# Performance work log

Hardware: AMD Instinct MI355X
Metric: run time of the kernel (lower is better)

Reference implementation:

```python
import jax, jax.numpy as jnp
import numpy as np

MODEL_DIM = 128
N_FRAMES = 128
N_SAMPLES = 32768
N_TABLES = 8
TABLE_SIZE = 512
BATCH = 8
N_FREQS = 16


def _mlp(x, w1, b1, w2, b2, w3, b3):
    # LinearOutputStack(channels, 3, ...): Linear -> lrelu -> Linear -> lrelu -> Linear
    h = jax.nn.leaky_relu(x @ w1 + b1, 0.2)
    h = jax.nn.leaky_relu(h @ w2 + b2, 0.2)
    return h @ w3 + b3


def _pos_encoded(t, n_freqs=N_FREQS):
    # (t, 1 + 2*n_freqs) = (t, 33): raw position plus sin/cos at geometric freqs
    pos = jnp.linspace(-1.0, 1.0, t, dtype=jnp.float32)
    scales = (2.0 ** jnp.arange(n_freqs, dtype=jnp.float32)) * jnp.pi
    ang = pos[:, None] * scales[None, :]
    return jnp.concatenate([pos[:, None], jnp.sin(ang), jnp.cos(ang)], axis=-1)


def _interp_linear(env, out_size):
    # torch F.interpolate(mode='linear', align_corners=False) from (B, F) to (B, out_size)
    f = env.shape[-1]
    coord = (jnp.arange(out_size, dtype=jnp.float32) + 0.5) * (f / out_size) - 0.5
    i0 = jnp.floor(coord)
    frac = (coord - i0).astype(env.dtype)
    i0c = jnp.clip(i0, 0, f - 1).astype(jnp.int32)
    i1c = jnp.clip(i0 + 1, 0, f - 1).astype(jnp.int32)
    return env[:, i0c] * (1.0 - frac) + env[:, i1c] * frac


def setup_inputs() -> dict:
    key = jax.random.key(0)
    ks = jax.random.split(key, 16)
    wi = 0.02  # weight_init from Experiment
    d = MODEL_DIM

    def lin(k, i, o):
        return jax.random.normal(k, (i, o), jnp.float32) * wi

    inp = {
        "x": jax.random.normal(ks[0], (BATCH, d), jnp.float32),
        "wavetables": jax.random.uniform(ks[1], (N_TABLES, TABLE_SIZE), jnp.float32, -1.0, 1.0),
    }
    specs = {"tc": (d, N_TABLES), "env": (d, N_FRAMES), "pos": (33, d), "sk": (d, TABLE_SIZE)}
    i = 2
    for name, (cin, cout) in specs.items():
        k1, k2, k3 = jax.random.split(ks[i], 3)
        inp[f"{name}_w1"] = lin(k1, cin, d)
        inp[f"{name}_b1"] = jnp.zeros((d,), jnp.float32)
        inp[f"{name}_w2"] = lin(k2, d, d)
        inp[f"{name}_b2"] = jnp.zeros((d,), jnp.float32)
        inp[f"{name}_w3"] = lin(k3, d, cout)
        inp[f"{name}_b3"] = jnp.zeros((cout,), jnp.float32)
        i += 1
    return inp


def reference(x, wavetables,
              tc_w1, tc_b1, tc_w2, tc_b2, tc_w3, tc_b3,
              env_w1, env_b1, env_w2, env_b2, env_w3, env_b3,
              pos_w1, pos_b1, pos_w2, pos_b2, pos_w3, pos_b3,
              sk_w1, sk_b1, sk_w2, sk_b2, sk_w3, sk_b3):
    # table choice: softmax then hard max (straight value * gathered table)
    c = jax.nn.softmax(_mlp(x, tc_w1, tc_b1, tc_w2, tc_b2, tc_w3, tc_b3), axis=-1)
    values = jnp.max(c, axis=-1)          # (B,)
    indices = jnp.argmax(c, axis=-1)      # (B,)

    mx = jnp.max(wavetables, axis=-1, keepdims=True)
    wt = wavetables / (mx + 1e-8)
    sel = wt[indices]                     # (B, TABLE_SIZE)

    env = jnp.abs(_mlp(x, env_w1, env_b1, env_w2, env_b2, env_w3, env_b3))  # (B, N_FRAMES)
    env = _interp_linear(env, N_SAMPLES)  # (B, N_SAMPLES)

    # pos encoding is identical across batch; embed once then broadcast (same math)
    pe = _pos_encoded(N_SAMPLES)          # (T, 33)
    pos = _mlp(pe, pos_w1, pos_b1, pos_w2, pos_b2, pos_w3, pos_b3)  # (T, D)
    pos = pos[None, :, :] + x[:, None, :]  # (B, T, D)

    sk = jax.nn.softmax(_mlp(pos, sk_w1, sk_b1, sk_w2, sk_b2, sk_w3, sk_b3), axis=-1)  # (B, T, K)

    # selected_tables (B,1,K) @ kernel^T (B,K,T) -> (B,1,T)
    sampled = jnp.einsum('bk,btk->bt', sel, sk)
    sampled = sampled * env * values[:, None]
    return sampled[:, None, :]
```

## Files before the change

### kernel.cpp

```cpp
#include <hip/hip_runtime.h>
#include <math.h>

#define D 128
#define B 8
#define T_SAMP 32768
#define K 512
#define NT 8
#define NFRM 128

#define WS_C1   0
#define WS_ENV8 1024
#define WS_SEL  2048
#define WS_VAL  6144
#define WS_B3P  6160
#define WSBF_BYTE 32768
#define FP1 0
#define FP2 8192
#define FP3 24576
#define FS1 40960
#define FS2 57344
#define FS3 73728
#define WTOT 139264
#define WS_NEED (WSBF_BYTE + WTOT*2)

typedef __attribute__((ext_vector_type(8))) short short8;
typedef __attribute__((ext_vector_type(4))) float f32x4;

#define LOG2E 1.4426950408889634f

__device__ __forceinline__ float lrelu(float v){ return fmaxf(v, 0.2f*v); }

__device__ __forceinline__ unsigned cvtpk(float lo, float hi){
    unsigned r;
    asm("v_cvt_pk_bf16_f32 %0, %1, %2" : "=v"(r) : "v"(lo), "v"(hi));
    return r;
}
__device__ __forceinline__ unsigned short bfr(float f){
    unsigned u = __builtin_bit_cast(unsigned, f); u += 0x7fffu + ((u>>16)&1u);
    return (unsigned short)(u>>16);
}
__device__ __forceinline__ float bf2f(short s){
    unsigned u = ((unsigned)(unsigned short)s) << 16;
    return __builtin_bit_cast(float, u);
}
__device__ __forceinline__ float exp2fast(float x){
#if __has_builtin(__builtin_amdgcn_exp2f)
    return __builtin_amdgcn_exp2f(x);
#else
    return __expf(x*0.6931471805599453f);
#endif
}
__device__ __forceinline__ float sin_rev(float fr){
#if __has_builtin(__builtin_amdgcn_sinf)
    return __builtin_amdgcn_sinf(fr);
#else
    return __sinf(fr*6.283185307179586f);
#endif
}
__device__ __forceinline__ float cos_rev(float fr){
#if __has_builtin(__builtin_amdgcn_cosf)
    return __builtin_amdgcn_cosf(fr);
#else
    return __cosf(fr*6.283185307179586f);
#endif
}
__device__ __forceinline__ float pe_val(float pf, int j){
    if (j == 0) return pf;
    if (j > 32) return 0.f;
    const bool is_sin = (j <= 16);
    int e = is_sin ? (j + 125) : (j + 109);
    float sc = __builtin_bit_cast(float, ((unsigned)e) << 23);
    float u = pf * sc;
    float fr = u - floorf(u);
    return is_sin ? sin_rev(fr) : cos_rev(fr);
}

#define VMCNT0 asm volatile("s_waitcnt vmcnt(0)" ::: "memory")

__device__ void layer128(const float* __restrict__ in, const float* __restrict__ w,
                         const float* __restrict__ bias, float* __restrict__ outp,
                         int tid, int mode)
{
    int n = tid & 127, bg = tid >> 7;
    const float* i0 = in + (bg*4+0)*D;
    const float* i1 = in + (bg*4+1)*D;
    const float* i2 = in + (bg*4+2)*D;
    const float* i3 = in + (bg*4+3)*D;
    float bb = bias[n];
    float a0=bb,a1=bb,a2=bb,a3=bb;
    #pragma unroll 4
    for (int j=0;j<D;j++){
        float wv = w[j*D+n];
        a0 = fmaf(i0[j], wv, a0);
        a1 = fmaf(i1[j], wv, a1);
        a2 = fmaf(i2[j], wv, a2);
        a3 = fmaf(i3[j], wv, a3);
    }
    if (mode==0){ a0=lrelu(a0);a1=lrelu(a1);a2=lrelu(a2);a3=lrelu(a3); }
    else if (mode==1){ a0=fabsf(a0);a1=fabsf(a1);a2=fabsf(a2);a3=fabsf(a3); }
    outp[(bg*4+0)*D+n]=a0;
    outp[(bg*4+1)*D+n]=a1;
    outp[(bg*4+2)*D+n]=a2;
    outp[(bg*4+3)*D+n]=a3;
}

__global__ __launch_bounds__(256) void setup_kernel(
    const float* __restrict__ x, const float* __restrict__ wt,
    const float* __restrict__ tc_w1, const float* __restrict__ tc_b1,
    const float* __restrict__ tc_w2, const float* __restrict__ tc_b2,
    const float* __restrict__ tc_w3, const float* __restrict__ tc_b3,
    const float* __restrict__ env_w1, const float* __restrict__ env_b1,
    const float* __restrict__ env_w2, const float* __restrict__ env_b2,
    const float* __restrict__ env_w3, const float* __restrict__ env_b3,
    const float* __restrict__ sk_w1, const float* __restrict__ sk_b1,
    const float* __restrict__ pos_w1, const float* __restrict__ pos_w2,
    const float* __restrict__ pos_w3, const float* __restrict__ sk_w2,
    const float* __restrict__ sk_w3, const float* __restrict__ sk_b3,
    float* __restrict__ ws)
{
    __shared__ float xl[B*D], buf1[B*D], buf2[B*D];
    __shared__ float lgts[B*NT], pmax[NT*8], mxr[NT];
    __shared__ int idxl[B];
    int tid = threadIdx.x;

    if (blockIdx.x >= 2){
        int idx = (blockIdx.x - 2)*256 + tid;
        if (idx >= WTOT) return;
        unsigned short* wb = (unsigned short*)((char*)ws + WSBF_BYTE);
        int r; const float* Wp; int ncols = D; int nkt = 4; bool p1 = false;
        if (idx < FP2){ r = idx - FP1; Wp = pos_w1; nkt = 2; p1 = true; }
        else if (idx < FP3){ r = idx - FP2; Wp = pos_w2; }
        else if (idx < FS1){ r = idx - FP3; Wp = pos_w3; }
        else if (idx < FS2){ r = idx - FS1; Wp = sk_w1; }
        else if (idx < FS3){ r = idx - FS2; Wp = sk_w2; }
        else { r = idx - FS3; Wp = sk_w3; ncols = K; }
        int frag = r >> 9, lane = (r >> 3) & 63, e = r & 7;
        int nt2 = frag / nkt, kt = frag - nt2*nkt;
        int k = 32*kt + 8*(lane>>4) + e;
        int n = 16*nt2 + (lane&15);
        float v = (p1 && k >= 33) ? 0.f : Wp[k*ncols + n];
        wb[idx] = bfr(v);
        return;
    }

    for (int i=tid;i<B*D;i+=256) xl[i]=x[i];
    __syncthreads();

    if (blockIdx.x == 1){
        for (int i=tid;i<K;i+=256) ws[WS_B3P+i] = sk_b3[i]*LOG2E;
        layer128(xl, env_w1, env_b1, buf1, tid, 0);
        __syncthreads();
        layer128(buf1, env_w2, env_b2, buf2, tid, 0);
        __syncthreads();
        layer128(buf2, env_w3, env_b3, ws+WS_ENV8, tid, 1);
        layer128(xl, sk_w1, sk_b1, ws+WS_C1, tid, 2);
        return;
    }

    layer128(xl, tc_w1, tc_b1, buf1, tid, 0);
    __syncthreads();
    layer128(buf1, tc_w2, tc_b2, buf2, tid, 0);
    __syncthreads();
    if (tid < 64){
        int b = tid>>3, n = tid&7;
        float a = tc_b3[n];
        #pragma unroll 4
        for (int j=0;j<D;j++) a = fmaf(buf2[b*D+j], tc_w3[j*NT+n], a);
        lgts[b*NT+n] = a;
    } else if (tid < 128){
        int r = (tid-64)>>3, p = tid&7;
        float m = -1e30f;
        for (int k=p*64;k<p*64+64;k++) m = fmaxf(m, wt[r*K+k]);
        pmax[r*8+p] = m;
    }
    __syncthreads();
    if (tid < 8){
        int b = tid; float m = -1e30f; int idx = 0;
        for (int n=0;n<NT;n++){ float v = lgts[b*NT+n]; if (v > m){ m=v; idx=n; } }
        float S = 0.f;
        for (int n=0;n<NT;n++) S += expf(lgts[b*NT+n]-m);
        ws[WS_VAL+b] = 1.0f/S;
        idxl[b] = idx;
    } else if (tid < 16){
        int r = tid-8; float m = -1e30f;
        for (int p=0;p<8;p++) m = fmaxf(m, pmax[r*8+p]);
        mxr[r] = m;
    }
    __syncthreads();
    for (int o=tid;o<B*K;o+=256){
        int b = o>>9, k = o&(K-1);
        int id = idxl[b];
        ws[WS_SEL+o] = wt[id*K+k] / (mxr[id] + 1e-8f);
    }
}

template<int NKT_IN, bool ACT>
__device__ __forceinline__ void layerF(const short8* aw,
                                       const unsigned char* inb, unsigned char* outb,
                                       const float* biasp, int wv, int lg, int lc)
{
    const f32x4 z = {0.f,0.f,0.f,0.f};
    const int lane16 = (lg*16 + lc)*16;
    const int obase = ((wv>>1)<<10) + (((2*(wv&1) + (lg>>1))*16 + lc)<<4) + ((lg&1)<<3);
    f32x4 bb = z;
    if (biasp) bb = *(const f32x4*)(biasp + 16*wv + 4*lg);
    #pragma unroll
    for (int rt=0;rt<2;rt++){
        f32x4 d = z;
        #pragma unroll
        for (int kt=0;kt<NKT_IN;kt++){
            short8 bf = *(const short8*)(inb + ((rt*NKT_IN+kt)<<10) + lane16);
            d = __builtin_amdgcn_mfma_f32_16x16x32_bf16(aw[kt], bf, d, 0,0,0);
        }
        float o0 = d[0]+bb[0], o1 = d[1]+bb[1], o2 = d[2]+bb[2], o3 = d[3]+bb[3];
        if (ACT){ o0=lrelu(o0); o1=lrelu(o1); o2=lrelu(o2); o3=lrelu(o3); }
        uint2 u; u.x = cvtpk(o0,o1); u.y = cvtpk(o2,o3);
        *(uint2*)(outb + (rt<<12) + obase) = u;
    }
}

__global__ __launch_bounds__(512, 4) void synth7(
    const float* __restrict__ pos_b1, const float* __restrict__ pos_b2,
    const float* __restrict__ pos_b3, const float* __restrict__ sk_b2,
    const float* __restrict__ ws, float* __restrict__ out)
{
    __shared__ __align__(16) unsigned char lds[32768];
    unsigned char* abA = lds;
    unsigned char* abB = lds + 8192;
    unsigned char* PEb = abB;

    const int tid = threadIdx.x;
    const int wv = tid >> 6, lane = tid & 63, lg = lane >> 4, lc = lane & 15;
    const int lane16 = lane*16;
    const int t0 = blockIdx.x * 32;
    const unsigned short* wg16 = (const unsigned short*)((const char*)ws + WSBF_BYTE);
    const f32x4 z = {0.f,0.f,0.f,0.f};

    auto stage = [&](int elemoff, unsigned char* dst, int nchunks){
        const unsigned char* src = (const unsigned char*)(wg16 + elemoff);
        for (int c = wv; c < nchunks; c += 8)
            __builtin_amdgcn_global_load_lds(
                (const __attribute__((address_space(1))) unsigned int*)(src + (c<<10) + lane16),
                (__attribute__((address_space(3))) unsigned int*)(dst + (c<<10)), 16, 0, 0);
    };

    short8 aw1[2];
    #pragma unroll
    for (int kt=0;kt<2;kt++)
        aw1[kt] = *(const short8*)(wg16 + FP1 + ((wv*2+kt)<<9) + lane*8);
    for (int i = tid; i < 1024; i += 512){
        int r = i >> 5, p = i & 31;
        int j0 = 2*p;
        float pf = (float)(-1.0 + 2.0*(double)(t0+r)/32767.0);
        float v0 = pe_val(pf, j0);
        float v1 = pe_val(pf, j0+1);
        int kt = j0 >> 5, rem = j0 & 31;
        int by = (((r>>4)*2 + kt)<<10) + (((rem>>3)*16 + (r&15))<<4) + (rem&7)*2;
        *(unsigned*)(PEb + by) = cvtpk(v0, v1);
    }
    __syncthreads();

    short8 awn[4];
    #pragma unroll
    for (int kt=0;kt<4;kt++)
        awn[kt] = *(const short8*)(wg16 + FP2 + ((wv*4+kt)<<9) + lane*8);
    layerF<2,true>(aw1, PEb, abA, pos_b1, wv, lg, lc);
    __syncthreads();
    {
        short8 awp[4];
        #pragma unroll
        for (int kt=0;kt<4;kt++)
            awp[kt] = *(const short8*)(wg16 + FP3 + ((wv*4+kt)<<9) + lane*8);
        layerF<4,true>(awn, abA, abB, pos_b2, wv, lg, lc);
        #pragma unroll
        for (int kt=0;kt<4;kt++) awn[kt] = awp[kt];
    }
    __syncthreads();
    {
        short8 awp[4];
        #pragma unroll
        for (int kt=0;kt<4;kt++)
            awp[kt] = *(const short8*)(wg16 + FS1 + ((wv*4+kt)<<9) + lane*8);
        layerF<4,false>(awn, abB, abA, pos_b3, wv, lg, lc);
        #pragma unroll
        for (int kt=0;kt<4;kt++) awn[kt] = awp[kt];
    }
    __syncthreads();
    layerF<4,false>(awn, abA, abB, nullptr, wv, lg, lc);
    __syncthreads();

    stage(FS2, lds, 8);
    short8 hf[2][4];
    {
        const int b = lc & 7;
        const float* c1g = ws + WS_C1 + b*128;
        #pragma unroll
        for (int rtl=0;rtl<2;rtl++){
            int tl = 4*wv + 2*rtl + (lc>>3);
            int fr = tl >> 4, lrow = tl & 15;
            #pragma unroll
            for (int kt=0;kt<4;kt++){
                short8 a1v = *(const short8*)(abB + ((fr*4+kt)<<10) + ((lg*16+lrow)<<4));
                const float* cp = c1g + 32*kt + 8*lg;
                f32x4 c0 = *(const f32x4*)cp;
                f32x4 c1v = *(const f32x4*)(cp+4);
                float h[8];
                #pragma unroll
                for (int e=0;e<4;e++){
                    h[e]   = lrelu(bf2f(a1v[e])   + c0[e]);
                    h[4+e] = lrelu(bf2f(a1v[4+e]) + c1v[e]);
                }
                uint4 t4; t4.x=cvtpk(h[0],h[1]); t4.y=cvtpk(h[2],h[3]);
                t4.z=cvtpk(h[4],h[5]); t4.w=cvtpk(h[6],h[7]);
                hf[rtl][kt] = __builtin_bit_cast(short8, t4);
            }
        }
    }
    __syncthreads();

    {
        const unsigned char* src = (const unsigned char*)(wg16 + FS2);
        for (int c = 8 + wv; c < 32; c += 8)
            __builtin_amdgcn_global_load_lds(
                (const __attribute__((address_space(1))) unsigned int*)(src + (c<<10) + lane16),
                (__attribute__((address_space(3))) unsigned int*)(lds + (c<<10)), 16, 0, 0);
    }
    VMCNT0; __syncthreads();

    short8 h2B[2][4];
    {
        const int sA = (2*(lg&1))*16 + lc;
        const int sB = sA + 16;
        const bool hi = (lg>>1) != 0;
        __builtin_amdgcn_s_setprio(1);
        #pragma unroll
        for (int kt2=0; kt2<4; kt2++){
            unsigned dpk[2][2][2];
            #pragma unroll
            for (int p=0;p<2;p++){
                int n2t = 2*kt2+p;
                short8 aw[4];
                #pragma unroll
                for (int kt=0;kt<4;kt++)
                    aw[kt] = *(const short8*)(lds + ((n2t*4+kt)<<10) + lane16);
                f32x4 b2 = *(const f32x4*)(sk_b2 + 16*n2t + 4*lg);
                #pragma unroll
                for (int rtl=0;rtl<2;rtl++){
                    f32x4 d = z;
                    #pragma unroll
                    for (int kt=0;kt<4;kt++)
                        d = __builtin_amdgcn_mfma_f32_16x16x32_bf16(aw[kt], hf[rtl][kt], d, 0,0,0);
                    float o0=lrelu(d[0]+b2[0]), o1=lrelu(d[1]+b2[1]);
                    float o2=lrelu(d[2]+b2[2]), o3=lrelu(d[3]+b2[3]);
                    dpk[p][rtl][0] = cvtpk(o0,o1);
                    dpk[p][rtl][1] = cvtpk(o2,o3);
                }
            }
            #pragma unroll
            for (int rtl=0;rtl<2;rtl++){
                unsigned a0 = (unsigned)__shfl((int)dpk[0][rtl][0], sA, 64);
                unsigned b0 = (unsigned)__shfl((int)dpk[1][rtl][0], sA, 64);
                unsigned a1 = (unsigned)__shfl((int)dpk[0][rtl][1], sA, 64);
                unsigned b1 = (unsigned)__shfl((int)dpk[1][rtl][1], sA, 64);
                unsigned a2 = (unsigned)__shfl((int)dpk[0][rtl][0], sB, 64);
                unsigned b2u= (unsigned)__shfl((int)dpk[1][rtl][0], sB, 64);
                unsigned a3 = (unsigned)__shfl((int)dpk[0][rtl][1], sB, 64);
                unsigned b3u= (unsigned)__shfl((int)dpk[1][rtl][1], sB, 64);
                uint4 uu;
                uu.x = hi ? b0 : a0;  uu.y = hi ? b1 : a1;
                uu.z = hi ? b2u : a2; uu.w = hi ? b3u : a3;
                h2B[rtl][kt2] = __builtin_bit_cast(short8, uu);
            }
        }
        __builtin_amdgcn_s_setprio(0);
    }
    __syncthreads();

    float SSa[2], WWa[2];
    SSa[0]=0.f; SSa[1]=0.f; WWa[0]=0.f; WWa[1]=0.f;

    stage(FS3, lds, 16); VMCNT0; __syncthreads();
    const float* selg = ws + WS_SEL + (lc & 7)*512;
    const float* b3g  = ws + WS_B3P;
    for (int c=0;c<8;c++){
        const unsigned char* slot = lds + (c&1)*16384;
        if (c < 7) stage(FS3 + (c+1)*8192, lds + ((c+1)&1)*16384, 16);
        __builtin_amdgcn_s_setprio(1);
        #pragma unroll
        for (int nl=0;nl<4;nl++){
            int n3t = 4*c + nl;
            short8 bw[4];
            #pragma unroll
            for (int kt=0;kt<4;kt++)
                bw[kt] = *(const short8*)(slot + ((nl*4+kt)<<10) + lane16);
            f32x4 d3[2]; d3[0]=z; d3[1]=z;
            #pragma unroll
            for (int rtl=0;rtl<2;rtl++){
                #pragma unroll
                for (int kt=0;kt<4;kt++)
                    d3[rtl] = __builtin_amdgcn_mfma_f32_16x16x32_bf16(bw[kt], h2B[rtl][kt], d3[rtl], 0,0,0);
            }
            f32x4 b3 = *(const f32x4*)(b3g + 16*n3t + 4*lg);
            f32x4 sv = *(const f32x4*)(selg + 16*n3t + 4*lg);
            #pragma unroll
            for (int rtl=0;rtl<2;rtl++){
                float e0 = exp2fast(fmaf(d3[rtl][0], LOG2E, b3[0]));
                float e1 = exp2fast(fmaf(d3[rtl][1], LOG2E, b3[1]));
                float e2 = exp2fast(fmaf(d3[rtl][2], LOG2E, b3[2]));
                float e3 = exp2fast(fmaf(d3[rtl][3], LOG2E, b3[3]));
                SSa[rtl] += (e0+e1) + (e2+e3);
                float w = fmaf(e0, sv[0], fmaf(e1, sv[1], fmaf(e2, sv[2], e3*sv[3])));
                WWa[rtl] += w;
            }
        }
        __builtin_amdgcn_s_setprio(0);
        VMCNT0; __syncthreads();
    }

    #pragma unroll
    for (int rtl=0;rtl<2;rtl++){
        float s = SSa[rtl];
        float w = WWa[rtl];
        s += __shfl_xor(s, 16, 64); s += __shfl_xor(s, 32, 64);
        w += __shfl_xor(w, 16, 64); w += __shfl_xor(w, 32, 64);
        if (lg == 0){
            int tl = 4*wv + 2*rtl + (lc>>3);
            int b  = lc & 7;
            int t  = t0 + tl;
            float coord = (t + 0.5f)*(1.0f/256.0f) - 0.5f;
            float fi = floorf(coord); float frac = coord - fi;
            int i0 = (int)fi; int i1 = i0 + 1;
            i0 = min(max(i0,0),NFRM-1); i1 = min(max(i1,0),NFRM-1);
            float e0 = ws[WS_ENV8 + b*NFRM + i0], e1 = ws[WS_ENV8 + b*NFRM + i1];
            float envv = e0*(1.0f-frac) + e1*frac;
            out[b*T_SAMP + t] = (w/s) * envv * ws[WS_VAL+b];
        }
    }
}

extern "C" void kernel_launch(void* const* d_in, const int* in_sizes, int n_in,
                              void* d_out, int out_size, void* d_ws, size_t ws_size,
                              hipStream_t stream)
{
    (void)in_sizes; (void)n_in; (void)out_size;
    const float* x       = (const float*)d_in[0];
    const float* wt      = (const float*)d_in[1];
    const float* tc_w1   = (const float*)d_in[2];
    const float* tc_b1   = (const float*)d_in[3];
    const float* tc_w2   = (const float*)d_in[4];
    const float* tc_b2   = (const float*)d_in[5];
    const float* tc_w3   = (const float*)d_in[6];
    const float* tc_b3   = (const float*)d_in[7];
    const float* env_w1  = (const float*)d_in[8];
    const float* env_b1  = (const float*)d_in[9];
    const float* env_w2  = (const float*)d_in[10];
    const float* env_b2  = (const float*)d_in[11];
    const float* env_w3  = (const float*)d_in[12];
    const float* env_b3  = (const float*)d_in[13];
    const float* pos_w1  = (const float*)d_in[14];
    const float* pos_b1  = (const float*)d_in[15];
    const float* pos_w2  = (const float*)d_in[16];
    const float* pos_b2  = (const float*)d_in[17];
    const float* pos_w3  = (const float*)d_in[18];
    const float* pos_b3  = (const float*)d_in[19];
    const float* sk_w1   = (const float*)d_in[20];
    const float* sk_b1   = (const float*)d_in[21];
    const float* sk_w2   = (const float*)d_in[22];
    const float* sk_b2   = (const float*)d_in[23];
    const float* sk_w3   = (const float*)d_in[24];
    const float* sk_b3   = (const float*)d_in[25];
    float* ws  = (float*)d_ws;
    float* out = (float*)d_out;

    if (ws_size < (size_t)WS_NEED) return;

    hipLaunchKernelGGL(setup_kernel, dim3(2 + (WTOT+255)/256), dim3(256), 0, stream,
        x, wt, tc_w1, tc_b1, tc_w2, tc_b2, tc_w3, tc_b3,
        env_w1, env_b1, env_w2, env_b2, env_w3, env_b3,
        sk_w1, sk_b1, pos_w1, pos_w2, pos_w3, sk_w2, sk_w3, sk_b3, ws);

    hipLaunchKernelGGL(synth7, dim3(T_SAMP/32), dim3(512), 0, stream,
        pos_b1, pos_b2, pos_b3, sk_b2, ws, out);
}
```

Baseline: 92.03 us.

## Process 64 time steps per block to reuse staged sk weights

Each block now handles two 32-sample halves instead of one. It runs the pos MLP for each half in turn, stores both layer-1 outputs in extra LDS, and then streams the sk layer-2/3 weights through LDS once for both halves. This halves the number of blocks and the per-block cost of staging the weight matrices. The cost is more LDS per block (40KB), more live registers (two h2B sets plus twice the accumulators), and possibly lower occupancy.

```diff
diff --git a/kernel.cpp b/kernel.cpp
--- a/kernel.cpp
+++ b/kernel.cpp
@@ -219,20 +219,22 @@
     }
 }
 
-__global__ __launch_bounds__(512, 4) void synth7(
+__global__ __launch_bounds__(512, 4) void synth8(
     const float* __restrict__ pos_b1, const float* __restrict__ pos_b2,
     const float* __restrict__ pos_b3, const float* __restrict__ sk_b2,
     const float* __restrict__ ws, float* __restrict__ out)
 {
-    __shared__ __align__(16) unsigned char lds[32768];
+    __shared__ __align__(16) unsigned char lds[40960];
     unsigned char* abA = lds;
     unsigned char* abB = lds + 8192;
     unsigned char* PEb = abB;
+    unsigned char* A1_0 = lds + 16384;
+    unsigned char* A1_1 = lds + 32768;
 
     const int tid = threadIdx.x;
     const int wv = tid >> 6, lane = tid & 63, lg = lane >> 4, lc = lane & 15;
     const int lane16 = lane*16;
-    const int t0 = blockIdx.x * 32;
+    const int t0 = blockIdx.x * 64;
     const unsigned short* wg16 = (const unsigned short*)((const char*)ws + WSBF_BYTE);
     const f32x4 z = {0.f,0.f,0.f,0.f};
 
@@ -244,94 +246,91 @@
                 (__attribute__((address_space(3))) unsigned int*)(dst + (c<<10)), 16, 0, 0);
     };
 
-    short8 aw1[2];
-    #pragma unroll
-    for (int kt=0;kt<2;kt++)
-        aw1[kt] = *(const short8*)(wg16 + FP1 + ((wv*2+kt)<<9) + lane*8);
-    for (int i = tid; i < 1024; i += 512){
-        int r = i >> 5, p = i & 31;
-        int j0 = 2*p;
-        float pf = (float)(-1.0 + 2.0*(double)(t0+r)/32767.0);
-        float v0 = pe_val(pf, j0);
-        float v1 = pe_val(pf, j0+1);
-        int kt = j0 >> 5, rem = j0 & 31;
-        int by = (((r>>4)*2 + kt)<<10) + (((rem>>3)*16 + (r&15))<<4) + (rem&7)*2;
-        *(unsigned*)(PEb + by) = cvtpk(v0, v1);
-    }
-    __syncthreads();
-
-    short8 awn[4];
-    #pragma unroll
-    for (int kt=0;kt<4;kt++)
-        awn[kt] = *(const short8*)(wg16 + FP2 + ((wv*4+kt)<<9) + lane*8);
-    layerF<2,true>(aw1, PEb, abA, pos_b1, wv, lg, lc);
-    __syncthreads();
-    {
-        short8 awp[4];
+    #pragma unroll 1
+    for (int h = 0; h < 2; ++h){
+        int t0h = t0 + 32*h;
+        for (int i = tid; i < 1024; i += 512){
+            int r = i >> 5, p = i & 31;
+            int j0 = 2*p;
+            float pf = (float)(-1.0 + 2.0*(double)(t0h+r)/32767.0);
+            float v0 = pe_val(pf, j0);
+            float v1 = pe_val(pf, j0+1);
+            int kt = j0 >> 5, rem = j0 & 31;
+            int by = (((r>>4)*2 + kt)<<10) + (((rem>>3)*16 + (r&15))<<4) + (rem&7)*2;
+            *(unsigned*)(PEb + by) = cvtpk(v0, v1);
+        }
+        __syncthreads();
+
+        short8 aw1[2];
+        #pragma unroll
+        for (int kt=0;kt<2;kt++)
+            aw1[kt] = *(const short8*)(wg16 + FP1 + ((wv*2+kt)<<9) + lane*8);
+        short8 awn[4];
         #pragma unroll
         for (int kt=0;kt<4;kt++)
-            awp[kt] = *(const short8*)(wg16 + FP3 + ((wv*4+kt)<<9) + lane*8);
-        layerF<4,true>(awn, abA, abB, pos_b2, wv, lg, lc);
-        #pragma unroll
-        for (int kt=0;kt<4;kt++) awn[kt] = awp[kt];
-    }
-    __syncthreads();
-    {
-        short8 awp[4];
-        #pragma unroll
-        for (int kt=0;kt<4;kt++)
-            awp[kt] = *(const short8*)(wg16 + FS1 + ((wv*4+kt)<<9) + lane*8);
-        layerF<4,false>(awn, abB, abA, pos_b3, wv, lg, lc);
-        #pragma unroll
-        for (int kt=0;kt<4;kt++) awn[kt] = awp[kt];
-    }
-    __syncthreads();
-    layerF<4,false>(awn, abA, abB, nullptr, wv, lg, lc);
-    __syncthreads();
-
-    stage(FS2, lds, 8);
-    short8 hf[2][4];
-    {
-        const int b = lc & 7;
-        const float* c1g = ws + WS_C1 + b*128;
+            awn[kt] = *(const short8*)(wg16 + FP2 + ((wv*4+kt)<<9) + lane*8);
+        layerF<2,true>(aw1, PEb, abA, pos_b1, wv, lg, lc);
+        __syncthreads();
+        {
+            short8 awp[4];
+            #pragma unroll
+            for (int kt=0;kt<4;kt++)
+                awp[kt] = *(const short8*)(wg16 + FP3 + ((wv*4+kt)<<9) + lane*8);
+            layerF<4,true>(awn, abA, abB, pos_b2, wv, lg, lc);
+            #pragma unroll
+            for (int kt=0;kt<4;kt++) awn[kt] = awp[kt];
+        }
+        __syncthreads();
+        {
+            short8 awp[4];
+            #pragma unroll
+            for (int kt=0;kt<4;kt++)
+                awp[kt] = *(const short8*)(wg16 + FS1 + ((wv*4+kt)<<9) + lane*8);
+            layerF<4,false>(awn, abB, abA, pos_b3, wv, lg, lc);
+            #pragma unroll
+            for (int kt=0;kt<4;kt++) awn[kt] = awp[kt];
+        }
+        __syncthreads();
+        layerF<4,false>(awn, abA, (h==0)?A1_0:A1_1, nullptr, wv, lg, lc);
+        __syncthreads();
+    }
+
+    const int bq = lc & 7;
+    const float* c1g = ws + WS_C1 + bq*128;
+    auto h1build = [&](const unsigned char* a1buf, short8 hf[2][4]){
         #pragma unroll
         for (int rtl=0;rtl<2;rtl++){
             int tl = 4*wv + 2*rtl + (lc>>3);
             int fr = tl >> 4, lrow = tl & 15;
             #pragma unroll
             for (int kt=0;kt<4;kt++){
-                short8 a1v = *(const short8*)(abB + ((fr*4+kt)<<10) + ((lg*16+lrow)<<4));
+                short8 a1v = *(const short8*)(a1buf + ((fr*4+kt)<<10) + ((lg*16+lrow)<<4));
                 const float* cp = c1g + 32*kt + 8*lg;
                 f32x4 c0 = *(const f32x4*)cp;
                 f32x4 c1v = *(const f32x4*)(cp+4);
-                float h[8];
+                float hh[8];
                 #pragma unroll
                 for (int e=0;e<4;e++){
-                    h[e]   = lrelu(bf2f(a1v[e])   + c0[e]);
-                    h[4+e] = lrelu(bf2f(a1v[4+e]) + c1v[e]);
+                    hh[e]   = lrelu(bf2f(a1v[e])   + c0[e]);
+                    hh[4+e] = lrelu(bf2f(a1v[4+e]) + c1v[e]);
                 }
-                uint4 t4; t4.x=cvtpk(h[0],h[1]); t4.y=cvtpk(h[2],h[3]);
-                t4.z=cvtpk(h[4],h[5]); t4.w=cvtpk(h[6],h[7]);
+                uint4 t4; t4.x=cvtpk(hh[0],hh[1]); t4.y=cvtpk(hh[2],hh[3]);
+                t4.z=cvtpk(hh[4],hh[5]); t4.w=cvtpk(hh[6],hh[7]);
                 hf[rtl][kt] = __builtin_bit_cast(short8, t4);
             }
         }
-    }
-    __syncthreads();
-
-    {
-        const unsigned char* src = (const unsigned char*)(wg16 + FS2);
-        for (int c = 8 + wv; c < 32; c += 8)
-            __builtin_amdgcn_global_load_lds(
-                (const __attribute__((address_space(1))) unsigned int*)(src + (c<<10) + lane16),
-                (__attribute__((address_space(3))) unsigned int*)(lds + (c<<10)), 16, 0, 0);
-    }
+    };
+
+    short8 hf[2][4];
+    h1build(A1_0, hf);
+    __syncthreads();
+    stage(FS2, lds, 32);
     VMCNT0; __syncthreads();
 
-    short8 h2B[2][4];
-    {
-        const int sA = (2*(lg&1))*16 + lc;
-        const int sB = sA + 16;
-        const bool hi = (lg>>1) != 0;
+    const int sA = (2*(lg&1))*16 + lc;
+    const int sB = sA + 16;
+    const bool hi = (lg>>1) != 0;
+    auto l2run = [&](const short8 hfin[2][4], short8 h2B[2][4]){
         __builtin_amdgcn_s_setprio(1);
         #pragma unroll
         for (int kt2=0; kt2<4; kt2++){
@@ -349,7 +348,7 @@
                     f32x4 d = z;
                     #pragma unroll
                     for (int kt=0;kt<4;kt++)
-                        d = __builtin_amdgcn_mfma_f32_16x16x32_bf16(aw[kt], hf[rtl][kt], d, 0,0,0);
+                        d = __builtin_amdgcn_mfma_f32_16x16x32_bf16(aw[kt], hfin[rtl][kt], d, 0,0,0);
                     float o0=lrelu(d[0]+b2[0]), o1=lrelu(d[1]+b2[1]);
                     float o2=lrelu(d[2]+b2[2]), o3=lrelu(d[3]+b2[3]);
                     dpk[p][rtl][0] = cvtpk(o0,o1);
@@ -373,14 +372,20 @@
             }
         }
         __builtin_amdgcn_s_setprio(0);
-    }
-    __syncthreads();
-
-    float SSa[2], WWa[2];
-    SSa[0]=0.f; SSa[1]=0.f; WWa[0]=0.f; WWa[1]=0.f;
+    };
+
+    short8 h2B0[2][4], h2B1[2][4];
+    l2run(hf, h2B0);
+    h1build(A1_1, hf);
+    l2run(hf, h2B1);
+    __syncthreads();
+
+    float SS0[2], WW0[2], SS1[2], WW1[2];
+    SS0[0]=SS0[1]=WW0[0]=WW0[1]=0.f;
+    SS1[0]=SS1[1]=WW1[0]=WW1[1]=0.f;
 
     stage(FS3, lds, 16); VMCNT0; __syncthreads();
-    const float* selg = ws + WS_SEL + (lc & 7)*512;
+    const float* selg = ws + WS_SEL + bq*512;
     const float* b3g  = ws + WS_B3P;
     for (int c=0;c<8;c++){
         const unsigned char* slot = lds + (c&1)*16384;
@@ -393,24 +398,32 @@
             #pragma unroll
             for (int kt=0;kt<4;kt++)
                 bw[kt] = *(const short8*)(slot + ((nl*4+kt)<<10) + lane16);
-            f32x4 d3[2]; d3[0]=z; d3[1]=z;
+            f32x4 d30[2], d31[2];
+            d30[0]=z; d30[1]=z; d31[0]=z; d31[1]=z;
             #pragma unroll
             for (int rtl=0;rtl<2;rtl++){
                 #pragma unroll
-                for (int kt=0;kt<4;kt++)
-                    d3[rtl] = __builtin_amdgcn_mfma_f32_16x16x32_bf16(bw[kt], h2B[rtl][kt], d3[rtl], 0,0,0);
+                for (int kt=0;kt<4;kt++){
+                    d30[rtl] = __builtin_amdgcn_mfma_f32_16x16x32_bf16(bw[kt], h2B0[rtl][kt], d30[rtl], 0,0,0);
+                    d31[rtl] = __builtin_amdgcn_mfma_f32_16x16x32_bf16(bw[kt], h2B1[rtl][kt], d31[rtl], 0,0,0);
+                }
             }
             f32x4 b3 = *(const f32x4*)(b3g + 16*n3t + 4*lg);
             f32x4 sv = *(const f32x4*)(selg + 16*n3t + 4*lg);
             #pragma unroll
             for (int rtl=0;rtl<2;rtl++){
-                float e0 = exp2fast(fmaf(d3[rtl][0], LOG2E, b3[0]));
-                float e1 = exp2fast(fmaf(d3[rtl][1], LOG2E, b3[1]));
-                float e2 = exp2fast(fmaf(d3[rtl][2], LOG2E, b3[2]));
-                float e3 = exp2fast(fmaf(d3[rtl][3], LOG2E, b3[3]));
-                SSa[rtl] += (e0+e1) + (e2+e3);
-                float w = fmaf(e0, sv[0], fmaf(e1, sv[1], fmaf(e2, sv[2], e3*sv[3])));
-                WWa[rtl] += w;
+                float e0 = exp2fast(fmaf(d30[rtl][0], LOG2E, b3[0]));
+                float e1 = exp2fast(fmaf(d30[rtl][1], LOG2E, b3[1]));
+                float e2 = exp2fast(fmaf(d30[rtl][2], LOG2E, b3[2]));
+                float e3 = exp2fast(fmaf(d30[rtl][3], LOG2E, b3[3]));
+                SS0[rtl] += (e0+e1) + (e2+e3);
+                WW0[rtl] += fmaf(e0, sv[0], fmaf(e1, sv[1], fmaf(e2, sv[2], e3*sv[3])));
+                float f0 = exp2fast(fmaf(d31[rtl][0], LOG2E, b3[0]));
+                float f1 = exp2fast(fmaf(d31[rtl][1], LOG2E, b3[1]));
+                float f2 = exp2fast(fmaf(d31[rtl][2], LOG2E, b3[2]));
+                float f3 = exp2fast(fmaf(d31[rtl][3], LOG2E, b3[3]));
+                SS1[rtl] += (f0+f1) + (f2+f3);
+                WW1[rtl] += fmaf(f0, sv[0], fmaf(f1, sv[1], fmaf(f2, sv[2], f3*sv[3])));
             }
         }
         __builtin_amdgcn_s_setprio(0);
@@ -418,22 +431,24 @@
     }
 
     #pragma unroll
-    for (int rtl=0;rtl<2;rtl++){
-        float s = SSa[rtl];
-        float w = WWa[rtl];
-        s += __shfl_xor(s, 16, 64); s += __shfl_xor(s, 32, 64);
-        w += __shfl_xor(w, 16, 64); w += __shfl_xor(w, 32, 64);
-        if (lg == 0){
-            int tl = 4*wv + 2*rtl + (lc>>3);
-            int b  = lc & 7;
-            int t  = t0 + tl;
-            float coord = (t + 0.5f)*(1.0f/256.0f) - 0.5f;
-            float fi = floorf(coord); float frac = coord - fi;
-            int i0 = (int)fi; int i1 = i0 + 1;
-            i0 = min(max(i0,0),NFRM-1); i1 = min(max(i1,0),NFRM-1);
-            float e0 = ws[WS_ENV8 + b*NFRM + i0], e1 = ws[WS_ENV8 + b*NFRM + i1];
-            float envv = e0*(1.0f-frac) + e1*frac;
-            out[b*T_SAMP + t] = (w/s) * envv * ws[WS_VAL+b];
+    for (int h2=0; h2<2; ++h2){
+        #pragma unroll
+        for (int rtl=0;rtl<2;rtl++){
+            float s = h2 ? SS1[rtl] : SS0[rtl];
+            float w = h2 ? WW1[rtl] : WW0[rtl];
+            s += __shfl_xor(s, 16, 64); s += __shfl_xor(s, 32, 64);
+            w += __shfl_xor(w, 16, 64); w += __shfl_xor(w, 32, 64);
+            if (lg == 0){
+                int tl = 4*wv + 2*rtl + (lc>>3);
+                int t  = t0 + 32*h2 + tl;
+                float coord = (t + 0.5f)*(1.0f/256.0f) - 0.5f;
+                float fi = floorf(coord); float frac = coord - fi;
+                int i0 = (int)fi; int i1 = i0 + 1;
+                i0 = min(max(i0,0),NFRM-1); i1 = min(max(i1,0),NFRM-1);
+                float e0 = ws[WS_ENV8 + bq*NFRM + i0], e1 = ws[WS_ENV8 + bq*NFRM + i1];
+                float envv = e0*(1.0f-frac) + e1*frac;
+                out[bq*T_SAMP + t] = (w/s) * envv * ws[WS_VAL+bq];
+            }
         }
     }
 }
@@ -479,6 +494,6 @@
         env_w1, env_b1, env_w2, env_b2, env_w3, env_b3,
         sk_w1, sk_b1, pos_w1, pos_w2, pos_w3, sk_w2, sk_w3, sk_b3, ws);
 
-    hipLaunchKernelGGL(synth7, dim3(T_SAMP/32), dim3(512), 0, stream,
+    hipLaunchKernelGGL(synth8, dim3(T_SAMP/64), dim3(512), 0, stream,
         pos_b1, pos_b2, pos_b3, sk_b2, ws, out);
 }
```

New measurement: 112.7 us. 22.4% more time.
